# Performance work log

Hardware: AMD Instinct MI355X
Metric: run time of the kernel (lower is better)

Reference implementation:

```python
import jax, jax.numpy as jnp
import numpy as np

K = 7            # kernel_size (odd, neighborhood width)
H = 16           # num_heads
DIM = 512        # model dim
D = DIM // H     # head_dim = 32
SCALE = D ** (-0.5)


def setup_inputs() -> dict:
    key = jax.random.key(0)
    k0, k1, k2, k3 = jax.random.split(key, 4)
    B, L, C = 2, 16384, DIM
    x = jax.random.normal(k0, (B, L, C), jnp.float32)
    qkv_w = jax.random.normal(k1, (3 * C, C), jnp.float32) * 0.02   # torch Linear weight [out, in]
    qkv_b = jnp.zeros((3 * C,), jnp.float32)
    rpb = jax.random.normal(k2, (H, 2 * K - 1), jnp.float32) * 0.02  # relative positional bias table
    proj_w = jax.random.normal(k3, (C, C), jnp.float32) * 0.02
    proj_b = jnp.zeros((C,), jnp.float32)
    return {"x": x, "qkv_w": qkv_w, "qkv_b": qkv_b, "rpb": rpb,
            "proj_w": proj_w, "proj_b": proj_b}


def reference(x, qkv_w, qkv_b, rpb, proj_w, proj_b):
    B, L, C = x.shape
    # qkv projection: [B, L, 3C] -> [3, B, H, L, D]
    qkv = (x @ qkv_w.T + qkv_b).reshape(B, L, 3, H, D).transpose(2, 0, 3, 1, 4)
    q = qkv[0] * SCALE
    k = qkv[1]
    v = qkv[2]

    # Neighborhood window start per query (clamped at boundaries, NATTEN semantics)
    pos = jnp.arange(L)
    ni = jnp.clip(pos - K // 2, 0, L - K)            # [L]
    idx = ni[:, None] + jnp.arange(K)                 # [L, K] key indices per query

    kg = k[:, :, idx]                                 # [B, H, L, K, D] gathered keys
    vg = v[:, :, idx]                                 # [B, H, L, K, D] gathered values

    # relative positional bias: rpb index = (j - i) + (K - 1)
    bias = rpb[:, idx - pos[:, None] + (K - 1)]       # [H, L, K]

    attn = jnp.einsum('bhld,bhlkd->bhlk', q, kg) + bias[None]
    attn = jax.nn.softmax(attn, axis=-1)              # softmax over the K-neighborhood
    out = jnp.einsum('bhlk,bhlkd->bhld', attn, vg)
    out = out.transpose(0, 2, 1, 3).reshape(B, L, C)
    return out @ proj_w.T + proj_b
```

## Files before the change

kernel.cpp:

```cpp
#include <hip/hip_runtime.h>

typedef unsigned short u16;
typedef unsigned int   u32;
typedef __attribute__((ext_vector_type(8))) short bf16x8;
typedef __attribute__((ext_vector_type(4))) float f32x4;

#define L_SEQ 16384
#define NHEAD 16
#define CDIM  512
#define SCALE 0.17677669529663689f

__device__ __forceinline__ float bf2f(u16 v) {
    union { u32 u; float f; } x; x.u = ((u32)v) << 16; return x.f;
}
__device__ __forceinline__ u16 f2bf(float f) {
    union { u32 u; float f; } x; x.f = f;
    u32 r = x.u + 0x7fff + ((x.u >> 16) & 1);
    return (u16)(r >> 16);
}

__global__ void detect_dtype_kernel(const u16* __restrict__ x, int* __restrict__ flag) {
    __shared__ int cnt;
    if (threadIdx.x == 0) cnt = 0;
    __syncthreads();
    int c = 0;
    for (int k = 0; k < 32; k++) {
        u16 v = x[2 * (threadIdx.x + 256 * k)];
        if ((v & 0x7F80) == 0x7F80) c++;
    }
    atomicAdd(&cnt, c);
    __syncthreads();
    if (threadIdx.x == 0) *flag = (cnt > 0) ? 1 : 0;
}

__global__ __launch_bounds__(256)
void convert_weights_kernel(const void* __restrict__ qkv_w, const void* __restrict__ proj_w,
                            const void* __restrict__ qkv_b, const void* __restrict__ proj_b,
                            const void* __restrict__ rpb, u16* __restrict__ dst,
                            const int* __restrict__ flag) {
    const int f = *flag;
    for (int i = blockIdx.x * 256 + threadIdx.x; i < 1050832; i += gridDim.x * 256) {
        const void* src; int off;
        if (i < 786432)       { src = qkv_w;  off = i; }
        else if (i < 1048576) { src = proj_w; off = i - 786432; }
        else if (i < 1050112) { src = qkv_b;  off = i - 1048576; }
        else if (i < 1050624) { src = proj_b; off = i - 1050112; }
        else                  { src = rpb;    off = i - 1050624; }
        dst[i] = f ? f2bf(((const float*)src)[off]) : ((const u16*)src)[off];
    }
}

__global__ __launch_bounds__(256)
void convert_x_kernel(const void* __restrict__ src, u16* __restrict__ dst,
                      int base_c, int lch, const int* __restrict__ flag) {
    const int f  = *flag;
    const int i0 = (blockIdx.x * 256 + threadIdx.x) * 8;
    const int r  = i0 >> 9;
    const int b  = (r >= lch) ? 1 : 0;
    const size_t s = (size_t)(b * L_SEQ + base_c + (r - b * lch)) * 512 + (i0 & 511);
    if (f) {
        const float* sf = (const float*)src + s;
        union { u16 o[8]; uint4 v; } pk;
        #pragma unroll
        for (int j = 0; j < 8; j++) pk.o[j] = f2bf(sf[j]);
        *(uint4*)(dst + i0) = pk.v;
    } else {
        *(uint4*)(dst + i0) = *(const uint4*)((const u16*)src + s);
    }
}

#define GEMM_CORE(A_PTR, W_PTR, KD, AROW0, N0)                                             \
    __shared__ u16 As[128 * 32];                                                           \
    __shared__ u16 Ws[128 * 32];                                                           \
    const int tid  = threadIdx.x;                                                          \
    const int wave = tid >> 6;                                                             \
    const int lane = tid & 63;                                                             \
    const int quad = lane >> 4;                                                            \
    const int r16  = lane & 15;                                                            \
    const int wm   = (wave >> 1) << 6;                                                     \
    const int wn   = (wave & 1) << 6;                                                      \
    f32x4 acc[4][4];                                                                       \
    _Pragma("unroll")                                                                      \
    for (int i = 0; i < 4; i++)                                                            \
        _Pragma("unroll")                                                                  \
        for (int j = 0; j < 4; j++) acc[i][j] = (f32x4){0.f, 0.f, 0.f, 0.f};               \
    const int srow = lane >> 2;                                                            \
    const int scol = (lane & 3) << 3;                                                      \
    u16* asb0 = As + wave * 512;                                                           \
    u16* asb1 = As + 2048 + wave * 512;                                                    \
    u16* wsb0 = Ws + wave * 512;                                                           \
    u16* wsb1 = Ws + 2048 + wave * 512;                                                    \
    const u16* ga = (A_PTR) + (size_t)((AROW0) + wave * 16 + srow) * (KD) + scol;          \
    const u16* gw = (W_PTR) + (size_t)((N0) + wave * 16 + srow) * (KD) + scol;             \
    for (int kt = 0; kt < (KD); kt += 32) {                                                \
        __builtin_amdgcn_global_load_lds(                                                  \
            (const __attribute__((address_space(1))) void*)(ga + kt),                      \
            (__attribute__((address_space(3))) void*)asb0, 16, 0, 0);                      \
        __builtin_amdgcn_global_load_lds(                                                  \
            (const __attribute__((address_space(1))) void*)(ga + (size_t)64 * (KD) + kt),  \
            (__attribute__((address_space(3))) void*)asb1, 16, 0, 0);                      \
        __builtin_amdgcn_global_load_lds(                                                  \
            (const __attribute__((address_space(1))) void*)(gw + kt),                      \
            (__attribute__((address_space(3))) void*)wsb0, 16, 0, 0);                      \
        __builtin_amdgcn_global_load_lds(                                                  \
            (const __attribute__((address_space(1))) void*)(gw + (size_t)64 * (KD) + kt),  \
            (__attribute__((address_space(3))) void*)wsb1, 16, 0, 0);                      \
        __syncthreads();                                                                   \
        bf16x8 af[4], bfr[4];                                                              \
        _Pragma("unroll")                                                                  \
        for (int mi = 0; mi < 4; mi++)                                                     \
            af[mi] = *(const bf16x8*)&As[(wm + mi * 16 + r16) * 32 + quad * 8];            \
        _Pragma("unroll")                                                                  \
        for (int ni = 0; ni < 4; ni++)                                                     \
            bfr[ni] = *(const bf16x8*)&Ws[(wn + ni * 16 + r16) * 32 + quad * 8];           \
        _Pragma("unroll")                                                                  \
        for (int mi = 0; mi < 4; mi++)                                                     \
            _Pragma("unroll")                                                              \
            for (int ni = 0; ni < 4; ni++)                                                 \
                acc[mi][ni] = __builtin_amdgcn_mfma_f32_16x16x32_bf16(                     \
                    af[mi], bfr[ni], acc[mi][ni], 0, 0, 0);                                \
        __syncthreads();                                                                   \
    }

__global__ __launch_bounds__(256)
void gemm_qkv_kernel(const u16* __restrict__ A, const u16* __restrict__ W,
                     const u16* __restrict__ bias, u16* __restrict__ qkv_out, int lch)
{
    const int m0l = blockIdx.x << 7;
    const int n0  = blockIdx.y << 7;
    const int b   = blockIdx.z;
    const size_t plane = (size_t)1024 * lch;
    GEMM_CORE(A, W, 512, b * lch + m0l, n0)
    #pragma unroll
    for (int ni = 0; ni < 4; ni++) {
        const int col   = n0 + wn + ni * 16 + r16;
        const int which = col >> 9;
        const int rem   = col & 511;
        const int h     = rem >> 5;
        const int d     = rem & 31;
        const float bv  = bf2f(bias[col]);
        const float scl = (which == 0) ? SCALE : 1.0f;
        u16* outb = qkv_out + (size_t)which * plane;
        #pragma unroll
        for (int mi = 0; mi < 4; mi++) {
            #pragma unroll
            for (int r = 0; r < 4; r++) {
                const int rrel = m0l + wm + mi * 16 + quad * 4 + r;
                outb[((size_t)(b * NHEAD + h) * lch + rrel) * 32 + d] =
                    f2bf((acc[mi][ni][r] + bv) * scl);
            }
        }
    }
}

__global__ __launch_bounds__(256)
void attn_kernel(const u32* __restrict__ q, const u32* __restrict__ k,
                 const u32* __restrict__ v, const u16* __restrict__ rpb,
                 u32* __restrict__ outa, int c0, int base_c, int lc_shift, int lch)
{
    const int grp = blockIdx.x * 16 + (threadIdx.x >> 4);
    const int d2  = threadIdx.x & 15;
    const int lc_mask = (1 << lc_shift) - 1;
    const int lr  = grp & lc_mask;
    const int bh  = grp >> lc_shift;
    const int h   = bh & 15;
    const int l   = c0 + lr;
    const size_t base = (size_t)bh * lch * 16;

    const u32 qp = q[base + (size_t)(l - base_c) * 16 + d2];
    const float qlo = bf2f((u16)qp), qhi = bf2f((u16)(qp >> 16));
    int ni = l - 3;
    if (ni < 0) ni = 0;
    if (ni > L_SEQ - 7) ni = L_SEQ - 7;
    const int rn = ni - base_c;

    float logit[7];
    #pragma unroll
    for (int j = 0; j < 7; j++) {
        const u32 kp = k[base + (size_t)(rn + j) * 16 + d2];
        float p = qlo * bf2f((u16)kp) + qhi * bf2f((u16)(kp >> 16));
        #pragma unroll
        for (int m = 8; m >= 1; m >>= 1) p += __shfl_xor(p, m, 64);
        logit[j] = p + bf2f(rpb[h * 13 + (ni + j - l + 6)]);
    }
    float mx = logit[0];
    #pragma unroll
    for (int j = 1; j < 7; j++) mx = fmaxf(mx, logit[j]);
    float s = 0.f, w[7];
    #pragma unroll
    for (int j = 0; j < 7; j++) { w[j] = __expf(logit[j] - mx); s += w[j]; }
    const float inv = 1.0f / s;
    float olo = 0.f, ohi = 0.f;
    #pragma unroll
    for (int j = 0; j < 7; j++) {
        const u32 vp = v[base + (size_t)(rn + j) * 16 + d2];
        olo += w[j] * bf2f((u16)vp);
        ohi += w[j] * bf2f((u16)(vp >> 16));
    }
    const u32 pk = (u32)f2bf(olo * inv) | ((u32)f2bf(ohi * inv) << 16);
    outa[((size_t)(((bh >> 4) << lc_shift) + lr)) * 256 + h * 16 + d2] = pk;
}

__global__ __launch_bounds__(256)
void gemm_proj_kernel(const u16* __restrict__ A, const u16* __restrict__ W,
                      const u16* __restrict__ bias, void* __restrict__ out,
                      int c0, int lc, const int* __restrict__ flag)
{
    const int m0l = blockIdx.x << 7;
    const int n0  = blockIdx.y << 7;
    const int b   = blockIdx.z;
    GEMM_CORE(A, W, 512, b * lc + m0l, n0)
    const int f = *flag;
    #pragma unroll
    for (int ni = 0; ni < 4; ni++) {
        const int col  = n0 + wn + ni * 16 + r16;
        const float bv = bf2f(bias[col]);
        #pragma unroll
        for (int mi = 0; mi < 4; mi++) {
            #pragma unroll
            for (int r = 0; r < 4; r++) {
                const int lr = m0l + wm + mi * 16 + quad * 4 + r;
                const size_t idx = (size_t)(b * L_SEQ + c0 + lr) * CDIM + col;
                const float val = acc[mi][ni][r] + bv;
                if (f) ((float*)out)[idx] = val;
                else   ((u16*)out)[idx]   = f2bf(val);
            }
        }
    }
}

extern "C" void kernel_launch(void* const* d_in, const int* in_sizes, int n_in,
                              void* d_out, int out_size, void* d_ws, size_t ws_size,
                              hipStream_t stream) {
    const void* x      = d_in[0];
    const void* qkv_w  = d_in[1];
    const void* qkv_b  = d_in[2];
    const void* rpb    = d_in[3];
    const void* proj_w = d_in[4];
    const void* proj_b = d_in[5];

    int nchunk, lch, lc, lc_shift;
    static const int c0sA[1] = {0},                 basesA[1] = {0};
    static const int c0sB[2] = {0, 8192},           basesB[2] = {0, 8064};
    static const int c0sC[8] = {0, 2048, 4096, 6144, 8192, 10240, 12288, 14336};
    static const int basesC[8] = {0, 1984, 4032, 6080, 8128, 10176, 12224, 14208};
    const int* c0s; const int* bases;
    if (ws_size >= (size_t)2 * (16 + 1050880 + (size_t)4096 * 16384 + 1024 * 16384)) {
        nchunk = 1; lch = 16384; lc = 16384; lc_shift = 14; c0s = c0sA; bases = basesA;
    } else if (ws_size >= (size_t)2 * (16 + 1050880 + (size_t)4096 * 8320 + 1024 * 8192)) {
        nchunk = 2; lch = 8320;  lc = 8192;  lc_shift = 13; c0s = c0sB; bases = basesB;
    } else {
        nchunk = 8; lch = 2176;  lc = 2048;  lc_shift = 11; c0s = c0sC; bases = basesC;
    }

    u16* ws    = (u16*)d_ws;
    int* flag  = (int*)ws;
    u16* wseg  = ws + 16;
    u16* wqkv  = wseg;
    u16* wproj = wseg + 786432;
    u16* bqkv  = wseg + 1048576;
    u16* bproj = wseg + 1050112;
    u16* rpbc  = wseg + 1050624;
    u16* xc    = ws + 16 + 1050880;
    u16* qkv   = xc + (size_t)1024 * lch;
    u16* wsa   = qkv + (size_t)3072 * lch;

    detect_dtype_kernel<<<1, 256, 0, stream>>>((const u16*)x, flag);
    convert_weights_kernel<<<2048, 256, 0, stream>>>(qkv_w, proj_w, qkv_b, proj_b,
                                                     rpb, wseg, flag);

    for (int c = 0; c < nchunk; c++) {
        convert_x_kernel<<<lch / 2, 256, 0, stream>>>(x, xc, bases[c], lch, flag);
        gemm_qkv_kernel<<<dim3(lch / 128, 12, 2), 256, 0, stream>>>(
            xc, wqkv, bqkv, qkv, lch);
        attn_kernel<<<2 * lc, 256, 0, stream>>>(
            (const u32*)qkv, (const u32*)(qkv + (size_t)1024 * lch),
            (const u32*)(qkv + (size_t)2048 * lch), rpbc,
            (u32*)wsa, c0s[c], bases[c], lc_shift, lch);
        gemm_proj_kernel<<<dim3(lc / 128, 4, 2), 256, 0, stream>>>(
            wsa, wproj, bproj, d_out, c0s[c], lc, flag);
    }
}
```

Measured before the change: 327.7 us.

## Double GEMM K-tile with XOR-swizzled LDS and vectorize attention loads

```diff
diff --git a/kernel.cpp b/kernel.cpp
--- a/kernel.cpp
+++ b/kernel.cpp
@@ -70,8 +70,8 @@
 }
 
 #define GEMM_CORE(A_PTR, W_PTR, KD, AROW0, N0)                                             \
-    __shared__ u16 As[128 * 32];                                                           \
-    __shared__ u16 Ws[128 * 32];                                                           \
+    __shared__ u16 As[128 * 64];                                                           \
+    __shared__ u16 Ws[128 * 64];                                                           \
     const int tid  = threadIdx.x;                                                          \
     const int wave = tid >> 6;                                                             \
     const int lane = tid & 63;                                                             \
@@ -84,41 +84,41 @@
     for (int i = 0; i < 4; i++)                                                            \
         _Pragma("unroll")                                                                  \
         for (int j = 0; j < 4; j++) acc[i][j] = (f32x4){0.f, 0.f, 0.f, 0.f};               \
-    const int srow = lane >> 2;                                                            \
-    const int scol = (lane & 3) << 3;                                                      \
-    u16* asb0 = As + wave * 512;                                                           \
-    u16* asb1 = As + 2048 + wave * 512;                                                    \
-    u16* wsb0 = Ws + wave * 512;                                                           \
-    u16* wsb1 = Ws + 2048 + wave * 512;                                                    \
-    const u16* ga = (A_PTR) + (size_t)((AROW0) + wave * 16 + srow) * (KD) + scol;          \
-    const u16* gw = (W_PTR) + (size_t)((N0) + wave * 16 + srow) * (KD) + scol;             \
-    for (int kt = 0; kt < (KD); kt += 32) {                                                \
-        __builtin_amdgcn_global_load_lds(                                                  \
-            (const __attribute__((address_space(1))) void*)(ga + kt),                      \
-            (__attribute__((address_space(3))) void*)asb0, 16, 0, 0);                      \
-        __builtin_amdgcn_global_load_lds(                                                  \
-            (const __attribute__((address_space(1))) void*)(ga + (size_t)64 * (KD) + kt),  \
-            (__attribute__((address_space(3))) void*)asb1, 16, 0, 0);                      \
-        __builtin_amdgcn_global_load_lds(                                                  \
-            (const __attribute__((address_space(1))) void*)(gw + kt),                      \
-            (__attribute__((address_space(3))) void*)wsb0, 16, 0, 0);                      \
-        __builtin_amdgcn_global_load_lds(                                                  \
-            (const __attribute__((address_space(1))) void*)(gw + (size_t)64 * (KD) + kt),  \
-            (__attribute__((address_space(3))) void*)wsb1, 16, 0, 0);                      \
+    const int lr8 = lane >> 3;                                                             \
+    const int swc = ((lane & 7) ^ lr8) << 3;                \
+    const u16* ga = (A_PTR) + (size_t)((AROW0) + wave * 8 + lr8) * (KD) + swc;             \
+    const u16* gw = (W_PTR) + (size_t)((N0) + wave * 8 + lr8) * (KD) + swc;                \
+    u16* asb = As + wave * 512;                                      \
+    u16* wsb = Ws + wave * 512;                                                            \
+    for (int kt = 0; kt < (KD); kt += 64) {                                                \
+        _Pragma("unroll")                                                                  \
+        for (int t = 0; t < 4; t++) {                                                      \
+            __builtin_amdgcn_global_load_lds(                                              \
+                (const __attribute__((address_space(1))) void*)(ga + kt + (size_t)(t * 32) * (KD)), \
+                (__attribute__((address_space(3))) void*)(asb + t * 2048), 16, 0, 0);      \
+            __builtin_amdgcn_global_load_lds(                                              \
+                (const __attribute__((address_space(1))) void*)(gw + kt + (size_t)(t * 32) * (KD)), \
+                (__attribute__((address_space(3))) void*)(wsb + t * 2048), 16, 0, 0);      \
+        }                                                                                  \
         __syncthreads();                                                                   \
-        bf16x8 af[4], bfr[4];                                                              \
         _Pragma("unroll")                                                                  \
-        for (int mi = 0; mi < 4; mi++)                                                     \
-            af[mi] = *(const bf16x8*)&As[(wm + mi * 16 + r16) * 32 + quad * 8];            \
-        _Pragma("unroll")                                                                  \
-        for (int ni = 0; ni < 4; ni++)                                                     \
-            bfr[ni] = *(const bf16x8*)&Ws[(wn + ni * 16 + r16) * 32 + quad * 8];           \
-        _Pragma("unroll")                                                                  \
-        for (int mi = 0; mi < 4; mi++)                                                     \
+        for (int ks = 0; ks < 2; ks++) {                                                   \
+            bf16x8 af[4], bfr[4];                                                          \
+            _Pragma("unroll")                                                              \
+            for (int mi = 0; mi < 4; mi++)                                                 \
+                af[mi] = *(const bf16x8*)&As[(wm + mi * 16 + r16) * 64 +                   \
+                                             (((ks * 4 + quad) ^ (r16 & 7)) << 3)];        \
             _Pragma("unroll")                                                              \
             for (int ni = 0; ni < 4; ni++)                                                 \
-                acc[mi][ni] = __builtin_amdgcn_mfma_f32_16x16x32_bf16(                     \
-                    af[mi], bfr[ni], acc[mi][ni], 0, 0, 0);                                \
+                bfr[ni] = *(const bf16x8*)&Ws[(wn + ni * 16 + r16) * 64 +                  \
+                                              (((ks * 4 + quad) ^ (r16 & 7)) << 3)];       \
+            _Pragma("unroll")                                                              \
+            for (int mi = 0; mi < 4; mi++)                                                 \
+                _Pragma("unroll")                                                          \
+                for (int ni = 0; ni < 4; ni++)                                             \
+                    acc[mi][ni] = __builtin_amdgcn_mfma_f32_16x16x32_bf16(                 \
+                        af[mi], bfr[ni], acc[mi][ni], 0, 0, 0);                            \
+        }                                                                                  \
         __syncthreads();                                                                   \
     }
 
@@ -154,21 +154,25 @@
 }
 
 __global__ __launch_bounds__(256)
-void attn_kernel(const u32* __restrict__ q, const u32* __restrict__ k,
-                 const u32* __restrict__ v, const u16* __restrict__ rpb,
-                 u32* __restrict__ outa, int c0, int base_c, int lc_shift, int lch)
+void attn_kernel(const uint4* __restrict__ q, const uint4* __restrict__ k,
+                 const uint4* __restrict__ v, const u16* __restrict__ rpb,
+                 uint4* __restrict__ outa, int c0, int base_c, int lc_shift, int lch)
 {
-    const int grp = blockIdx.x * 16 + (threadIdx.x >> 4);
-    const int d2  = threadIdx.x & 15;
-    const int lc_mask = (1 << lc_shift) - 1;
-    const int lr  = grp & lc_mask;
+    const int grp = blockIdx.x * 64 + (threadIdx.x >> 2);
+    const int d4  = threadIdx.x & 3;
+    const int lr  = grp & ((1 << lc_shift) - 1);
     const int bh  = grp >> lc_shift;
     const int h   = bh & 15;
     const int l   = c0 + lr;
-    const size_t base = (size_t)bh * lch * 16;
-
-    const u32 qp = q[base + (size_t)(l - base_c) * 16 + d2];
-    const float qlo = bf2f((u16)qp), qhi = bf2f((u16)(qp >> 16));
+    const size_t base = (size_t)bh * lch * 4;
+
+    const uint4 qp = q[base + (size_t)(l - base_c) * 4 + d4];
+    float qf[8];
+    qf[0] = bf2f((u16)qp.x); qf[1] = bf2f((u16)(qp.x >> 16));
+    qf[2] = bf2f((u16)qp.y); qf[3] = bf2f((u16)(qp.y >> 16));
+    qf[4] = bf2f((u16)qp.z); qf[5] = bf2f((u16)(qp.z >> 16));
+    qf[6] = bf2f((u16)qp.w); qf[7] = bf2f((u16)(qp.w >> 16));
+
     int ni = l - 3;
     if (ni < 0) ni = 0;
     if (ni > L_SEQ - 7) ni = L_SEQ - 7;
@@ -177,10 +181,14 @@
     float logit[7];
     #pragma unroll
     for (int j = 0; j < 7; j++) {
-        const u32 kp = k[base + (size_t)(rn + j) * 16 + d2];
-        float p = qlo * bf2f((u16)kp) + qhi * bf2f((u16)(kp >> 16));
-        #pragma unroll
-        for (int m = 8; m >= 1; m >>= 1) p += __shfl_xor(p, m, 64);
+        const uint4 kp = k[base + (size_t)(rn + j) * 4 + d4];
+        float p;
+        p  = qf[0] * bf2f((u16)kp.x) + qf[1] * bf2f((u16)(kp.x >> 16));
+        p += qf[2] * bf2f((u16)kp.y) + qf[3] * bf2f((u16)(kp.y >> 16));
+        p += qf[4] * bf2f((u16)kp.z) + qf[5] * bf2f((u16)(kp.z >> 16));
+        p += qf[6] * bf2f((u16)kp.w) + qf[7] * bf2f((u16)(kp.w >> 16));
+        p += __shfl_xor(p, 1, 64);
+        p += __shfl_xor(p, 2, 64);
         logit[j] = p + bf2f(rpb[h * 13 + (ni + j - l + 6)]);
     }
     float mx = logit[0];
@@ -190,15 +198,21 @@
     #pragma unroll
     for (int j = 0; j < 7; j++) { w[j] = __expf(logit[j] - mx); s += w[j]; }
     const float inv = 1.0f / s;
-    float olo = 0.f, ohi = 0.f;
+    float o[8] = {0.f, 0.f, 0.f, 0.f, 0.f, 0.f, 0.f, 0.f};
     #pragma unroll
     for (int j = 0; j < 7; j++) {
-        const u32 vp = v[base + (size_t)(rn + j) * 16 + d2];
-        olo += w[j] * bf2f((u16)vp);
-        ohi += w[j] * bf2f((u16)(vp >> 16));
-    }
-    const u32 pk = (u32)f2bf(olo * inv) | ((u32)f2bf(ohi * inv) << 16);
-    outa[((size_t)(((bh >> 4) << lc_shift) + lr)) * 256 + h * 16 + d2] = pk;
+        const uint4 vp = v[base + (size_t)(rn + j) * 4 + d4];
+        o[0] += w[j] * bf2f((u16)vp.x); o[1] += w[j] * bf2f((u16)(vp.x >> 16));
+        o[2] += w[j] * bf2f((u16)vp.y); o[3] += w[j] * bf2f((u16)(vp.y >> 16));
+        o[4] += w[j] * bf2f((u16)vp.z); o[5] += w[j] * bf2f((u16)(vp.z >> 16));
+        o[6] += w[j] * bf2f((u16)vp.w); o[7] += w[j] * bf2f((u16)(vp.w >> 16));
+    }
+    uint4 pk;
+    pk.x = (u32)f2bf(o[0] * inv) | ((u32)f2bf(o[1] * inv) << 16);
+    pk.y = (u32)f2bf(o[2] * inv) | ((u32)f2bf(o[3] * inv) << 16);
+    pk.z = (u32)f2bf(o[4] * inv) | ((u32)f2bf(o[5] * inv) << 16);
+    pk.w = (u32)f2bf(o[6] * inv) | ((u32)f2bf(o[7] * inv) << 16);
+    outa[((size_t)(((bh >> 4) << lc_shift) + lr)) * 64 + h * 4 + d4] = pk;
 }
 
 __global__ __launch_bounds__(256)
@@ -273,10 +287,10 @@
         convert_x_kernel<<<lch / 2, 256, 0, stream>>>(x, xc, bases[c], lch, flag);
         gemm_qkv_kernel<<<dim3(lch / 128, 12, 2), 256, 0, stream>>>(
             xc, wqkv, bqkv, qkv, lch);
-        attn_kernel<<<2 * lc, 256, 0, stream>>>(
-            (const u32*)qkv, (const u32*)(qkv + (size_t)1024 * lch),
-            (const u32*)(qkv + (size_t)2048 * lch), rpbc,
-            (u32*)wsa, c0s[c], bases[c], lc_shift, lch);
+        attn_kernel<<<lc / 2, 256, 0, stream>>>(
+            (const uint4*)qkv, (const uint4*)(qkv + (size_t)1024 * lch),
+            (const uint4*)(qkv + (size_t)2048 * lch), rpbc,
+            (uint4*)wsa, c0s[c], bases[c], lc_shift, lch);
         gemm_proj_kernel<<<dim3(lc / 128, 4, 2), 256, 0, stream>>>(
             wsa, wproj, bproj, d_out, c0s[c], lc, flag);
     }
```

Result: faster. 289.8 us (-11.6%).
